# Kernel optimization log

Hardware: AMD Instinct MI355X
Metric: run time of the kernel (lower is better)

## Reference

```python
import jax, jax.numpy as jnp
import numpy as np

N = 100000
E = 3200000
IN_DIM = 256
HID = 128
HID2 = 64
K = 16


def setup_inputs() -> dict:
    key = jax.random.key(0)
    ks = jax.random.split(key, 12)
    x = jax.random.normal(ks[0], (N, IN_DIM), dtype=jnp.float32)
    edge_index = jax.random.randint(ks[1], (2, E), 0, N, dtype=jnp.int64)
    edge_weight = jax.random.uniform(ks[2], (E,), dtype=jnp.float32)
    s = lambda f: 1.0 / np.sqrt(f)
    W0 = jax.random.normal(ks[3], (IN_DIM, HID), dtype=jnp.float32) * s(IN_DIM)
    b0 = jnp.zeros((HID,), jnp.float32)
    P0w = jax.random.normal(ks[4], (IN_DIM, HID), dtype=jnp.float32) * s(IN_DIM)
    P0b = jnp.zeros((HID,), jnp.float32)
    W1 = jax.random.normal(ks[5], (HID, HID2), dtype=jnp.float32) * s(HID)
    b1 = jnp.zeros((HID2,), jnp.float32)
    P1w = jax.random.normal(ks[6], (HID, HID2), dtype=jnp.float32) * s(HID)
    P1b = jnp.zeros((HID2,), jnp.float32)
    W2 = jax.random.normal(ks[7], (HID2, K), dtype=jnp.float32) * s(HID2)
    b2 = jnp.zeros((K,), jnp.float32)
    return {"x": x, "edge_index": edge_index, "edge_weight": edge_weight,
            "W0": W0, "b0": b0, "P0w": P0w, "P0b": P0b,
            "W1": W1, "b1": b1, "P1w": P1w, "P1b": P1b,
            "W2": W2, "b2": b2}


def _gcn_norm(edge_index, edge_weight, n):
    # add self loops (weight 1), symmetric normalization per PyG gcn_norm
    loop = jnp.arange(n, dtype=edge_index.dtype)
    row = jnp.concatenate([edge_index[0], loop])
    col = jnp.concatenate([edge_index[1], loop])
    w = jnp.concatenate([edge_weight, jnp.ones((n,), edge_weight.dtype)])
    deg = jax.ops.segment_sum(w, col, num_segments=n)
    dinv = jnp.where(deg > 0, jax.lax.rsqrt(deg), 0.0)
    return row, col, dinv[row] * w * dinv[col]


def reference(x, edge_index, edge_weight, W0, b0, P0w, P0b, W1, b1, P1w, P1b, W2, b2):
    n = x.shape[0]
    row, col, nw = _gcn_norm(edge_index, edge_weight, n)

    def gcn(h, W, b):
        hW = h @ W  # transform first (PyG GCNConv), then scatter-aggregate
        agg = jax.ops.segment_sum(nw[:, None] * hW[row], col, num_segments=n)
        return agg + b

    # layer 0: skip is Linear(input_dim, hidden); dropout = identity (eval)
    h = jax.nn.selu(gcn(x, W0, b0) + (x @ P0w + P0b))
    # layer 1: skip is Linear(hidden, hidden//2)
    h = jax.nn.selu(gcn(h, W1, b1) + (h @ P1w + P1b))
    # layer 2: no skip, no dropout
    h = jax.nn.selu(gcn(h, W2, b2))
    return jax.nn.softmax(h, axis=-1)
```

## Files before the change

### kernel.cpp

```cpp
#include <hip/hip_runtime.h>
#include <hip/hip_fp16.h>
#include <cmath>

#define IN_DIM 256
#define HID 128
#define HID2 64
#define SB 256
#define NODES_PB 128
#define NB_MAX 1024
#define BCAP 4608

struct __align__(8) EdgeP { int s; float w; };
union H4 { __half h[4]; uint2 u; };

using f16x8 = __attribute__((ext_vector_type(8))) _Float16;
using f32x4 = __attribute__((ext_vector_type(4))) float;

__device__ __forceinline__ float selu_f(float x) {
    const float scale = 1.0507009873554805f;
    const float alpha = 1.6732632423543772f;
    return x > 0.f ? scale * x : scale * alpha * expm1f(x);
}


__global__ void zero_ints(int* p, int n) {
    int i = blockIdx.x * blockDim.x + threadIdx.x;
    if (i < n) p[i] = 0;
}

__global__ void transpose_w(const float* __restrict__ B1, const float* __restrict__ B2,
                            __half* __restrict__ WT, int K, int C1, int C2) {
    int c = blockIdx.x;
    for (int k = threadIdx.x; k < K; k += blockDim.x) {
        float v = (c < C1) ? B1[(size_t)k * C1 + c] : B2[(size_t)k * C2 + (c - C1)];
        WT[(size_t)c * K + k] = __float2half(v);
    }
}

__global__ void deg_dinv(const EdgeP* __restrict__ ell, int* cnt, float* dinv, int n, int cap) {
    int wid = (blockIdx.x * blockDim.x + threadIdx.x) >> 6;
    int lane = threadIdx.x & 63;
    if (wid >= n) return;
    size_t base = (size_t)wid * cap;
    int len = min(cnt[wid], cap);
    float s = 0.f;
    for (int i = lane; i < len; i += 64) s += ell[base + i].w;
#pragma unroll
    for (int o = 32; o; o >>= 1) s += __shfl_xor(s, o);
    if (lane == 0) {
        dinv[wid] = rsqrtf(s + 1.0f);
        cnt[wid] = len;
    }
}

__global__ __launch_bounds__(256) void bin_gemm0(
    const float* __restrict__ A, const __half* __restrict__ WT,
    const float* __restrict__ bias1, const float* __restrict__ bias2,
    __half* __restrict__ outA, float* __restrict__ outB, int M,
    const int* __restrict__ ei, const float* __restrict__ ew,
    int* cnt_or_bcur, EdgeP* __restrict__ dst_buf,
    int E, int cap, int epb, int sblocks, int nb, int mode) {
    const int tid = threadIdx.x;
    __shared__ __align__(16) __half sA16[128 * 40];
    __shared__ __align__(16) __half sB16[128 * 40];

    if ((int)blockIdx.x < sblocks) {
        int lo = blockIdx.x * epb;
        int hi = min(E, lo + epb);
        if (mode == 1) {
            int* hist = (int*)sA16;
            int* gbase = (int*)sB16;
            for (int i = tid; i < nb; i += 256) hist[i] = 0;
            __syncthreads();
            for (int e = lo + tid; e < hi; e += 256)
                atomicAdd(&hist[ei[E + e] >> 7], 1);
            __syncthreads();
            for (int b = tid; b < nb; b += 256) {
                int h = hist[b];
                gbase[b] = h ? atomicAdd(&cnt_or_bcur[b], h) : 0;
                hist[b] = 0;
            }
            __syncthreads();
            for (int e = lo + tid; e < hi; e += 256) {
                int d = ei[E + e];
                int s = ei[e];
                float w = ew[e];
                int b = d >> 7;
                int lp = atomicAdd(&hist[b], 1);
                int off = gbase[b] + lp;
                if (off < BCAP) {
                    EdgeP p; p.s = (s << 7) | (d & 127); p.w = w;
                    dst_buf[(size_t)b * BCAP + off] = p;
                }
            }
        } else {
            for (int base = lo; base < hi; base += 2048) {
                int r[8], c[8], pos[8];
                float wv[8];
#pragma unroll
                for (int j = 0; j < 8; ++j) {
                    int e = base + j * 256 + tid;
                    c[j] = -1;
                    if (e < hi) { r[j] = ei[e]; c[j] = ei[E + e]; wv[j] = ew[e]; }
                }
#pragma unroll
                for (int j = 0; j < 8; ++j)
                    if (c[j] >= 0) pos[j] = atomicAdd(&cnt_or_bcur[c[j]], 1);
#pragma unroll
                for (int j = 0; j < 8; ++j)
                    if (c[j] >= 0 && pos[j] < cap) {
                        EdgeP p; p.s = r[j]; p.w = wv[j];
                        dst_buf[(size_t)c[j] * cap + pos[j]] = p;
                    }
            }
        }
        return;
    }

    const int bid = blockIdx.x - sblocks;
    const int m0 = (bid >> 1) * 128;
    const int n0 = (bid & 1) * 128;
    const int lane = tid & 63;
    const int wv = tid >> 6;
    const int wr = (wv >> 1) * 64;
    const int wc = (wv & 1) * 64;
    const int lr = lane & 15, lk = lane >> 4;

    f32x4 zero = {0.f, 0.f, 0.f, 0.f};
    f32x4 acc[4][4];
#pragma unroll
    for (int i = 0; i < 4; ++i)
#pragma unroll
        for (int j = 0; j < 4; ++j) acc[i][j] = zero;

    for (int k0 = 0; k0 < IN_DIM; k0 += 32) {
#pragma unroll
        for (int p = 0; p < 4; ++p) {
            int f4 = p * 256 + tid;
            int r = f4 >> 3;
            int kk = (f4 & 7) << 2;
            int row = m0 + r;
            float4 v = make_float4(0.f, 0.f, 0.f, 0.f);
            if (row < M) v = *(const float4*)(A + (size_t)row * IN_DIM + k0 + kk);
            H4 h;
            h.h[0] = __float2half(v.x); h.h[1] = __float2half(v.y);
            h.h[2] = __float2half(v.z); h.h[3] = __float2half(v.w);
            *(uint2*)&sA16[r * 40 + kk] = h.u;
        }
#pragma unroll
        for (int p = 0; p < 2; ++p) {
            int f = p * 256 + tid;
            int c = f >> 2;
            int kc = (f & 3) << 3;
            *(uint4*)&sB16[c * 40 + kc] =
                *(const uint4*)(WT + (size_t)(n0 + c) * IN_DIM + k0 + kc);
        }
        __syncthreads();
        f16x8 af[4], bf[4];
#pragma unroll
        for (int i = 0; i < 4; ++i)
            af[i] = *(const f16x8*)&sA16[(wr + i * 16 + lr) * 40 + lk * 8];
#pragma unroll
        for (int j = 0; j < 4; ++j)
            bf[j] = *(const f16x8*)&sB16[(wc + j * 16 + lr) * 40 + lk * 8];
#pragma unroll
        for (int i = 0; i < 4; ++i)
#pragma unroll
            for (int j = 0; j < 4; ++j)
                acc[i][j] = __builtin_amdgcn_mfma_f32_16x16x32_f16(af[i], bf[j], acc[i][j], 0, 0, 0);
        __syncthreads();
    }

    float bs[4];
    if (n0 != 0) {
#pragma unroll
        for (int j = 0; j < 4; ++j) {
            int c = wc + j * 16 + lr;
            bs[j] = bias1[c] + bias2[c];
        }
    }
#pragma unroll
    for (int i = 0; i < 4; ++i) {
        int rowb = m0 + wr + i * 16 + lk * 4;
#pragma unroll
        for (int j = 0; j < 4; ++j) {
            int col = wc + j * 16 + lr;
#pragma unroll
            for (int r = 0; r < 4; ++r) {
                int row = rowb + r;
                if (row < M) {
                    if (n0 == 0)
                        outA[(size_t)row * HID + col] = __float2half(acc[i][j][r]);
                    else
                        outB[(size_t)row * HID + col] = acc[i][j][r] + bs[j];
                }
            }
        }
    }
}

__global__ __launch_bounds__(256) void bucket_build(
    const EdgeP* __restrict__ recs, const int* __restrict__ bcur,
    EdgeP* __restrict__ ell, int* __restrict__ cnt, float* __restrict__ dinv,
    int n, int cap) {
    __shared__ int lcnt[NODES_PB];
    __shared__ float ldeg[NODES_PB];
    int b = blockIdx.x, tid = threadIdx.x;
    if (tid < NODES_PB) { lcnt[tid] = 0; ldeg[tid] = 0.f; }
    __syncthreads();
    int m = min(bcur[b], BCAP);
    const EdgeP* r = recs + (size_t)b * BCAP;
    for (int i = tid; i < m; i += 256) {
        EdgeP p = r[i];
        int dl = p.s & 127;
        int s = p.s >> 7;
        int pos = atomicAdd(&lcnt[dl], 1);
        atomicAdd(&ldeg[dl], p.w);
        if (pos < cap) {
            EdgeP q; q.s = s; q.w = p.w;
            ell[((size_t)(b * NODES_PB + dl)) * cap + pos] = q;
        }
    }
    __syncthreads();
    if (tid < NODES_PB) {
        int v = b * NODES_PB + tid;
        if (v < n) {
            cnt[v] = min(lcnt[tid], cap);
            dinv[v] = rsqrtf(ldeg[tid] + 1.0f);
        }
    }
}

__global__ __launch_bounds__(256) void gemm1_fused(
    const float* __restrict__ A, const __half* __restrict__ WT,
    const float* __restrict__ bias1, const float* __restrict__ bias2,
    __half* __restrict__ outA, float* __restrict__ outB, int M) {
    const int tid = threadIdx.x;
    __shared__ __align__(16) __half sA16[128 * 40];
    __shared__ __align__(16) __half sB16[128 * 40];
    const int m0 = blockIdx.x * 128;
    const int lane = tid & 63;
    const int wv = tid >> 6;
    const int wr = (wv >> 1) * 64;
    const int wc = (wv & 1) * 64;
    const int lr = lane & 15, lk = lane >> 4;

    f32x4 zero = {0.f, 0.f, 0.f, 0.f};
    f32x4 acc[4][4];
#pragma unroll
    for (int i = 0; i < 4; ++i)
#pragma unroll
        for (int j = 0; j < 4; ++j) acc[i][j] = zero;

    for (int k0 = 0; k0 < HID; k0 += 32) {
#pragma unroll
        for (int p = 0; p < 4; ++p) {
            int f4 = p * 256 + tid;
            int r = f4 >> 3;
            int kk = (f4 & 7) << 2;
            int row = m0 + r;
            float4 v = make_float4(0.f, 0.f, 0.f, 0.f);
            if (row < M) v = *(const float4*)(A + (size_t)row * HID + k0 + kk);
            H4 h;
            h.h[0] = __float2half(v.x); h.h[1] = __float2half(v.y);
            h.h[2] = __float2half(v.z); h.h[3] = __float2half(v.w);
            *(uint2*)&sA16[r * 40 + kk] = h.u;
        }
#pragma unroll
        for (int p = 0; p < 2; ++p) {
            int f = p * 256 + tid;
            int c = f >> 2;
            int kc = (f & 3) << 3;
            *(uint4*)&sB16[c * 40 + kc] =
                *(const uint4*)(WT + (size_t)c * HID + k0 + kc);
        }
        __syncthreads();
        f16x8 af[4], bf[4];
#pragma unroll
        for (int i = 0; i < 4; ++i)
            af[i] = *(const f16x8*)&sA16[(wr + i * 16 + lr) * 40 + lk * 8];
#pragma unroll
        for (int j = 0; j < 4; ++j)
            bf[j] = *(const f16x8*)&sB16[(wc + j * 16 + lr) * 40 + lk * 8];
#pragma unroll
        for (int i = 0; i < 4; ++i)
#pragma unroll
            for (int j = 0; j < 4; ++j)
                acc[i][j] = __builtin_amdgcn_mfma_f32_16x16x32_f16(af[i], bf[j], acc[i][j], 0, 0, 0);
        __syncthreads();
    }

    float bs[4];
    if (wc != 0) {
#pragma unroll
        for (int j = 0; j < 4; ++j) {
            int c = wc + j * 16 + lr - HID2;
            bs[j] = bias1[c] + bias2[c];
        }
    }
#pragma unroll
    for (int i = 0; i < 4; ++i) {
        int rowb = m0 + wr + i * 16 + lk * 4;
#pragma unroll
        for (int j = 0; j < 4; ++j) {
            int col = wc + j * 16 + lr;
#pragma unroll
            for (int r = 0; r < 4; ++r) {
                int row = rowb + r;
                if (row < M) {
                    if (wc == 0)
                        outA[(size_t)row * HID2 + col] = __float2half(acc[i][j][r]);
                    else
                        outB[(size_t)row * HID2 + (col - HID2)] = acc[i][j][r] + bs[j];
                }
            }
        }
    }
}

template <int F>
__global__ void aggregate(const __half* __restrict__ hW, float* __restrict__ S,
                          const float* __restrict__ dinv, const int* __restrict__ cnt,
                          const EdgeP* __restrict__ ell, int cap, int n) {
    int v = blockIdx.x;
    int f = threadIdx.x;
    float di = dinv[v];
    float self = S[(size_t)v * F + f] + di * di * __half2float(hW[(size_t)v * F + f]);
    size_t base = (size_t)v * cap;
    int len = cnt[v];
    float a0 = 0.f, a1 = 0.f, a2 = 0.f, a3 = 0.f;
    int i = 0;
    for (; i + 3 < len; i += 4) {
        EdgeP p0 = ell[base + i], p1 = ell[base + i + 1];
        EdgeP p2 = ell[base + i + 2], p3 = ell[base + i + 3];
        float t0 = dinv[p0.s] * p0.w, t1 = dinv[p1.s] * p1.w;
        float t2 = dinv[p2.s] * p2.w, t3 = dinv[p3.s] * p3.w;
        a0 = fmaf(t0, __half2float(hW[(size_t)p0.s * F + f]), a0);
        a1 = fmaf(t1, __half2float(hW[(size_t)p1.s * F + f]), a1);
        a2 = fmaf(t2, __half2float(hW[(size_t)p2.s * F + f]), a2);
        a3 = fmaf(t3, __half2float(hW[(size_t)p3.s * F + f]), a3);
    }
    for (; i < len; ++i) {
        EdgeP p = ell[base + i];
        a0 = fmaf(dinv[p.s] * p.w, __half2float(hW[(size_t)p.s * F + f]), a0);
    }
    float acc = self + di * ((a0 + a1) + (a2 + a3));
    S[(size_t)v * F + f] = selu_f(acc);
}

__global__ __launch_bounds__(256) void agg64_gemm2(
    const __half* __restrict__ hW, const float* __restrict__ S,
    const float* __restrict__ dinv, const int* __restrict__ cnt,
    const EdgeP* __restrict__ ell, int cap,
    const float* __restrict__ W2, __half* __restrict__ out16, int n) {
    __shared__ float sW[64 * 16];
    __shared__ float sh[4][64];
    int tid = threadIdx.x;
#pragma unroll
    for (int i = 0; i < 4; ++i) sW[i * 256 + tid] = W2[i * 256 + tid];

    int g = tid >> 6, f = tid & 63;
    int v = blockIdx.x * 4 + g;
    if (v < n) {
        float di = dinv[v];
        float self = S[(size_t)v * 64 + f] + di * di * __half2float(hW[(size_t)v * 64 + f]);
        size_t base = (size_t)v * cap;
        int len = cnt[v];
        float a0 = 0.f, a1 = 0.f, a2 = 0.f, a3 = 0.f;
        int i = 0;
        for (; i + 3 < len; i += 4) {
            EdgeP p0 = ell[base + i], p1 = ell[base + i + 1];
            EdgeP p2 = ell[base + i + 2], p3 = ell[base + i + 3];
            float t0 = dinv[p0.s] * p0.w, t1 = dinv[p1.s] * p1.w;
            float t2 = dinv[p2.s] * p2.w, t3 = dinv[p3.s] * p3.w;
            a0 = fmaf(t0, __half2float(hW[(size_t)p0.s * 64 + f]), a0);
            a1 = fmaf(t1, __half2float(hW[(size_t)p1.s * 64 + f]), a1);
            a2 = fmaf(t2, __half2float(hW[(size_t)p2.s * 64 + f]), a2);
            a3 = fmaf(t3, __half2float(hW[(size_t)p3.s * 64 + f]), a3);
        }
        for (; i < len; ++i) {
            EdgeP p = ell[base + i];
            a0 = fmaf(dinv[p.s] * p.w, __half2float(hW[(size_t)p.s * 64 + f]), a0);
        }
        sh[g][f] = selu_f(self + di * ((a0 + a1) + (a2 + a3)));
    }
    __syncthreads();
    if (v < n && f < 16) {
        float acc = 0.f;
#pragma unroll
        for (int k = 0; k < 64; ++k) acc = fmaf(sh[g][k], sW[k * 16 + f], acc);
        out16[(size_t)v * 16 + f] = __float2half(acc);
    }
}

__global__ void agg_softmax(const __half* __restrict__ hW, const float* __restrict__ b2,
                            const float* __restrict__ dinv, const int* __restrict__ cnt,
                            const EdgeP* __restrict__ ell, int cap,
                            float* __restrict__ out, int n) {
    int lane = threadIdx.x;
    int g = lane >> 4, f = lane & 15;
    int v = blockIdx.x * 4 + g;
    if (v >= n) return;
    float di = dinv[v];
    float acc = b2[f] + di * di * __half2float(hW[(size_t)v * 16 + f]);
    size_t base = (size_t)v * cap;
    int len = cnt[v];
    float a0 = 0.f;
    for (int i = 0; i < len; ++i) {
        EdgeP p = ell[base + i];
        a0 = fmaf(dinv[p.s] * p.w, __half2float(hW[(size_t)p.s * 16 + f]), a0);
    }
    acc += di * a0;
    acc = selu_f(acc);
    float m = acc;
    m = fmaxf(m, __shfl_xor(m, 1));
    m = fmaxf(m, __shfl_xor(m, 2));
    m = fmaxf(m, __shfl_xor(m, 4));
    m = fmaxf(m, __shfl_xor(m, 8));
    float ex = expf(acc - m);
    float sm = ex;
    sm += __shfl_xor(sm, 1);
    sm += __shfl_xor(sm, 2);
    sm += __shfl_xor(sm, 4);
    sm += __shfl_xor(sm, 8);
    out[(size_t)v * 16 + f] = ex / sm;
}

extern "C" void kernel_launch(void* const* d_in, const int* in_sizes, int n_in,
                              void* d_out, int out_size, void* d_ws, size_t ws_size,
                              hipStream_t stream) {
    const float* x = (const float*)d_in[0];
    const int* ei = (const int*)d_in[1];
    const float* ew = (const float*)d_in[2];
    const float* W0 = (const float*)d_in[3];
    const float* b0 = (const float*)d_in[4];
    const float* P0w = (const float*)d_in[5];
    const float* P0b = (const float*)d_in[6];
    const float* W1 = (const float*)d_in[7];
    const float* b1 = (const float*)d_in[8];
    const float* P1w = (const float*)d_in[9];
    const float* P1b = (const float*)d_in[10];
    const float* W2 = (const float*)d_in[11];
    const float* b2 = (const float*)d_in[12];
    float* out = (float*)d_out;
    const int n = in_sizes[0] / IN_DIM;
    const int E = in_sizes[2];
    const int NB = (n + NODES_PB - 1) / NODES_PB;

    auto al = [](size_t b) { return (b + 255) & ~(size_t)255; };
    size_t oCnt = 0;
    size_t oDinv = oCnt + al((size_t)n * 4);
    size_t oBcur = oDinv + al((size_t)n * 4);
    size_t oWT0 = oBcur + al((size_t)NB_MAX * 4);
    size_t oWT1 = oWT0 + al((size_t)IN_DIM * (HID * 2) * 2);
    size_t oA = oWT1 + al((size_t)HID * HID * 2);
    size_t oB = oA + al((size_t)n * HID * 2);
    size_t oEll = oB + al((size_t)n * HID * 4);
    size_t szEll96 = al((size_t)n * 96 * 8);
    size_t szEll80 = al((size_t)n * 80 * 8);
    size_t szRec = al((size_t)NB * BCAP * 8);
    size_t szCD = al((size_t)n * HID2 * 4) + al((size_t)n * 16 * 2);
    size_t szR = szRec > szCD ? szRec : szCD;

    int cap;
    int mode;
    if (NB <= NB_MAX && oEll + szEll96 + szR <= ws_size) { cap = 96; mode = 1; }
    else if (oEll + szEll96 + szCD <= ws_size) { cap = 96; mode = 0; }
    else { cap = 80; mode = 0; }

    char* base = (char*)d_ws;
    int* cnt = (int*)(base + oCnt);
    float* dinv = (float*)(base + oDinv);
    int* bcur = (int*)(base + oBcur);
    __half* WT0 = (__half*)(base + oWT0);
    __half* WT1 = (__half*)(base + oWT1);
    __half* bufA = (__half*)(base + oA);
    float* bufB = (float*)(base + oB);
    EdgeP* ell = (EdgeP*)(base + oEll);
    size_t oR = oEll + (cap == 96 ? szEll96 : szEll80);
    EdgeP* recs = (EdgeP*)(base + oR);
    float* bufC = (float*)(base + oR);
    __half* bufD = (__half*)(base + oR + al((size_t)n * HID2 * 4));

    int gx = (n + 127) / 128;
    int gemmBlocks = gx * 2;
    int epb = (E + SB - 1) / SB;

    transpose_w<<<2 * HID, 128, 0, stream>>>(W0, P0w, WT0, IN_DIM, HID, HID);
    transpose_w<<<HID, 128, 0, stream>>>(W1, P1w, WT1, HID, HID2, HID2);

    if (mode == 1) {
        zero_ints<<<(NB_MAX + 255) / 256, 256, 0, stream>>>(bcur, NB_MAX);
        bin_gemm0<<<SB + gemmBlocks, 256, 0, stream>>>(
            x, WT0, b0, P0b, bufA, bufB, n, ei, ew, bcur, recs,
            E, cap, epb, SB, NB, 1);
        bucket_build<<<NB, 256, 0, stream>>>(recs, bcur, ell, cnt, dinv, n, cap);
    } else {
        zero_ints<<<(n + 255) / 256, 256, 0, stream>>>(cnt, n);
        bin_gemm0<<<SB + gemmBlocks, 256, 0, stream>>>(
            x, WT0, b0, P0b, bufA, bufB, n, ei, ew, cnt, ell,
            E, cap, epb, SB, NB, 0);
        int nbW = (n * 64 + 255) / 256;
        deg_dinv<<<nbW, 256, 0, stream>>>(ell, cnt, dinv, n, cap);
    }

    aggregate<HID><<<n, HID, 0, stream>>>(bufA, bufB, dinv, cnt, ell, cap, n);

    gemm1_fused<<<gx, 256, 0, stream>>>(bufB, WT1, b1, P1b, bufA, bufC, n);

    agg64_gemm2<<<(n + 3) / 4, 256, 0, stream>>>(bufA, bufC, dinv, cnt, ell, cap, W2, bufD, n);
    agg_softmax<<<(n + 3) / 4, 64, 0, stream>>>(bufD, b2, dinv, cnt, ell, cap, out, n);
}
```

Measured before the change: 585.5 us.

## Restructure GCN aggregation kernels with wave-per-node half2 gathers and deeper unrolling

The layer-0 aggregation now assigns one 64-lane wavefront per node instead of a 128-thread block, and each lane handles two features through half2 loads and float2 stores. All three aggregation kernels unroll the edge loop by 8 (or 4), issuing every edge-record and neighbor-row load before the FMAs so more gathers are in flight. The softmax aggregation kernel now packs 16 nodes per 256-thread block instead of 4 per 64-thread block. The aim is more memory-level parallelism and fewer, wider transactions in these latency-bound gathers, at the cost of more registers.

```diff
diff --git a/kernel.cpp b/kernel.cpp
--- a/kernel.cpp
+++ b/kernel.cpp
@@ -12,6 +12,7 @@
 
 struct __align__(8) EdgeP { int s; float w; };
 union H4 { __half h[4]; uint2 u; };
+union H2 { __half2 h2; uint u; };
 
 using f16x8 = __attribute__((ext_vector_type(8))) _Float16;
 using f32x4 = __attribute__((ext_vector_type(4))) float;
@@ -318,34 +319,56 @@
     }
 }
 
-template <int F>
-__global__ void aggregate(const __half* __restrict__ hW, float* __restrict__ S,
-                          const float* __restrict__ dinv, const int* __restrict__ cnt,
-                          const EdgeP* __restrict__ ell, int cap, int n) {
-    int v = blockIdx.x;
-    int f = threadIdx.x;
+__global__ __launch_bounds__(256) void aggregate128(
+    const __half* __restrict__ hW, float* __restrict__ S,
+    const float* __restrict__ dinv, const int* __restrict__ cnt,
+    const EdgeP* __restrict__ ell, int cap, int n) {
+    int v = (blockIdx.x * 256 + threadIdx.x) >> 6;
+    int lane = threadIdx.x & 63;
+    if (v >= n) return;
     float di = dinv[v];
-    float self = S[(size_t)v * F + f] + di * di * __half2float(hW[(size_t)v * F + f]);
+    float2 sv = *(const float2*)&S[(size_t)v * HID + lane * 2];
+    H2 selfh; selfh.u = *(const uint*)&hW[(size_t)v * HID + lane * 2];
+    float2 selff = __half22float2(selfh.h2);
+    float selfx = sv.x + di * di * selff.x;
+    float selfy = sv.y + di * di * selff.y;
+
     size_t base = (size_t)v * cap;
     int len = cnt[v];
-    float a0 = 0.f, a1 = 0.f, a2 = 0.f, a3 = 0.f;
+    float ax[4] = {0.f, 0.f, 0.f, 0.f};
+    float ay[4] = {0.f, 0.f, 0.f, 0.f};
     int i = 0;
-    for (; i + 3 < len; i += 4) {
-        EdgeP p0 = ell[base + i], p1 = ell[base + i + 1];
-        EdgeP p2 = ell[base + i + 2], p3 = ell[base + i + 3];
-        float t0 = dinv[p0.s] * p0.w, t1 = dinv[p1.s] * p1.w;
-        float t2 = dinv[p2.s] * p2.w, t3 = dinv[p3.s] * p3.w;
-        a0 = fmaf(t0, __half2float(hW[(size_t)p0.s * F + f]), a0);
-        a1 = fmaf(t1, __half2float(hW[(size_t)p1.s * F + f]), a1);
-        a2 = fmaf(t2, __half2float(hW[(size_t)p2.s * F + f]), a2);
-        a3 = fmaf(t3, __half2float(hW[(size_t)p3.s * F + f]), a3);
+    for (; i + 8 <= len; i += 8) {
+        EdgeP p[8];
+        float dv[8];
+        uint h[8];
+#pragma unroll
+        for (int j = 0; j < 8; ++j) p[j] = ell[base + i + j];
+#pragma unroll
+        for (int j = 0; j < 8; ++j) {
+            dv[j] = dinv[p[j].s];
+            h[j] = *(const uint*)&hW[(size_t)p[j].s * HID + lane * 2];
+        }
+#pragma unroll
+        for (int j = 0; j < 8; ++j) {
+            float t = dv[j] * p[j].w;
+            H2 hh; hh.u = h[j];
+            float2 hf = __half22float2(hh.h2);
+            ax[j & 3] = fmaf(t, hf.x, ax[j & 3]);
+            ay[j & 3] = fmaf(t, hf.y, ay[j & 3]);
+        }
     }
     for (; i < len; ++i) {
         EdgeP p = ell[base + i];
-        a0 = fmaf(dinv[p.s] * p.w, __half2float(hW[(size_t)p.s * F + f]), a0);
-    }
-    float acc = self + di * ((a0 + a1) + (a2 + a3));
-    S[(size_t)v * F + f] = selu_f(acc);
+        float t = dinv[p.s] * p.w;
+        H2 hh; hh.u = *(const uint*)&hW[(size_t)p.s * HID + lane * 2];
+        float2 hf = __half22float2(hh.h2);
+        ax[0] = fmaf(t, hf.x, ax[0]);
+        ay[0] = fmaf(t, hf.y, ay[0]);
+    }
+    float sx = selfx + di * ((ax[0] + ax[1]) + (ax[2] + ax[3]));
+    float sy = selfy + di * ((ay[0] + ay[1]) + (ay[2] + ay[3]));
+    *(float2*)&S[(size_t)v * HID + lane * 2] = make_float2(selu_f(sx), selu_f(sy));
 }
 
 __global__ __launch_bounds__(256) void agg64_gemm2(
@@ -366,23 +389,28 @@
         float self = S[(size_t)v * 64 + f] + di * di * __half2float(hW[(size_t)v * 64 + f]);
         size_t base = (size_t)v * cap;
         int len = cnt[v];
-        float a0 = 0.f, a1 = 0.f, a2 = 0.f, a3 = 0.f;
+        float a[4] = {0.f, 0.f, 0.f, 0.f};
         int i = 0;
-        for (; i + 3 < len; i += 4) {
-            EdgeP p0 = ell[base + i], p1 = ell[base + i + 1];
-            EdgeP p2 = ell[base + i + 2], p3 = ell[base + i + 3];
-            float t0 = dinv[p0.s] * p0.w, t1 = dinv[p1.s] * p1.w;
-            float t2 = dinv[p2.s] * p2.w, t3 = dinv[p3.s] * p3.w;
-            a0 = fmaf(t0, __half2float(hW[(size_t)p0.s * 64 + f]), a0);
-            a1 = fmaf(t1, __half2float(hW[(size_t)p1.s * 64 + f]), a1);
-            a2 = fmaf(t2, __half2float(hW[(size_t)p2.s * 64 + f]), a2);
-            a3 = fmaf(t3, __half2float(hW[(size_t)p3.s * 64 + f]), a3);
+        for (; i + 8 <= len; i += 8) {
+            EdgeP p[8];
+            float dv[8];
+            __half hv[8];
+#pragma unroll
+            for (int j = 0; j < 8; ++j) p[j] = ell[base + i + j];
+#pragma unroll
+            for (int j = 0; j < 8; ++j) {
+                dv[j] = dinv[p[j].s];
+                hv[j] = hW[(size_t)p[j].s * 64 + f];
+            }
+#pragma unroll
+            for (int j = 0; j < 8; ++j)
+                a[j & 3] = fmaf(dv[j] * p[j].w, __half2float(hv[j]), a[j & 3]);
         }
         for (; i < len; ++i) {
             EdgeP p = ell[base + i];
-            a0 = fmaf(dinv[p.s] * p.w, __half2float(hW[(size_t)p.s * 64 + f]), a0);
-        }
-        sh[g][f] = selu_f(self + di * ((a0 + a1) + (a2 + a3)));
+            a[0] = fmaf(dinv[p.s] * p.w, __half2float(hW[(size_t)p.s * 64 + f]), a[0]);
+        }
+        sh[g][f] = selu_f(self + di * ((a[0] + a[1]) + (a[2] + a[3])));
     }
     __syncthreads();
     if (v < n && f < 16) {
@@ -393,24 +421,41 @@
     }
 }
 
-__global__ void agg_softmax(const __half* __restrict__ hW, const float* __restrict__ b2,
-                            const float* __restrict__ dinv, const int* __restrict__ cnt,
-                            const EdgeP* __restrict__ ell, int cap,
-                            float* __restrict__ out, int n) {
-    int lane = threadIdx.x;
-    int g = lane >> 4, f = lane & 15;
-    int v = blockIdx.x * 4 + g;
+__global__ __launch_bounds__(256) void agg_softmax(
+    const __half* __restrict__ hW, const float* __restrict__ b2,
+    const float* __restrict__ dinv, const int* __restrict__ cnt,
+    const EdgeP* __restrict__ ell, int cap,
+    float* __restrict__ out, int n) {
+    int tid = threadIdx.x;
+    int g = tid >> 4, f = tid & 15;
+    int v = blockIdx.x * 16 + g;
     if (v >= n) return;
     float di = dinv[v];
     float acc = b2[f] + di * di * __half2float(hW[(size_t)v * 16 + f]);
     size_t base = (size_t)v * cap;
     int len = cnt[v];
-    float a0 = 0.f;
-    for (int i = 0; i < len; ++i) {
+    float a[4] = {0.f, 0.f, 0.f, 0.f};
+    int i = 0;
+    for (; i + 4 <= len; i += 4) {
+        EdgeP p[4];
+        float dv[4];
+        __half hv[4];
+#pragma unroll
+        for (int j = 0; j < 4; ++j) p[j] = ell[base + i + j];
+#pragma unroll
+        for (int j = 0; j < 4; ++j) {
+            dv[j] = dinv[p[j].s];
+            hv[j] = hW[(size_t)p[j].s * 16 + f];
+        }
+#pragma unroll
+        for (int j = 0; j < 4; ++j)
+            a[j] = fmaf(dv[j] * p[j].w, __half2float(hv[j]), a[j]);
+    }
+    for (; i < len; ++i) {
         EdgeP p = ell[base + i];
-        a0 = fmaf(dinv[p.s] * p.w, __half2float(hW[(size_t)p.s * 16 + f]), a0);
-    }
-    acc += di * a0;
+        a[0] = fmaf(dinv[p.s] * p.w, __half2float(hW[(size_t)p.s * 16 + f]), a[0]);
+    }
+    acc += di * ((a[0] + a[1]) + (a[2] + a[3]));
     acc = selu_f(acc);
     float m = acc;
     m = fmaxf(m, __shfl_xor(m, 1));
@@ -504,10 +549,10 @@
         deg_dinv<<<nbW, 256, 0, stream>>>(ell, cnt, dinv, n, cap);
     }
 
-    aggregate<HID><<<n, HID, 0, stream>>>(bufA, bufB, dinv, cnt, ell, cap, n);
+    aggregate128<<<(n * 64 + 255) / 256, 256, 0, stream>>>(bufA, bufB, dinv, cnt, ell, cap, n);
 
     gemm1_fused<<<gx, 256, 0, stream>>>(bufB, WT1, b1, P1b, bufA, bufC, n);
 
     agg64_gemm2<<<(n + 3) / 4, 256, 0, stream>>>(bufA, bufC, dinv, cnt, ell, cap, W2, bufD, n);
-    agg_softmax<<<(n + 3) / 4, 64, 0, stream>>>(bufD, b2, dinv, cnt, ell, cap, out, n);
-}
+    agg_softmax<<<(n + 15) / 16, 256, 0, stream>>>(bufD, b2, dinv, cnt, ell, cap, out, n);
+}
```

After: 512.0 us. 12.6% less time.
